# Optimization experiments

Hardware: AMD Instinct MI355X
Metric: run time of the kernel (lower is better)

The kernel has to match this reference:

```python
import jax, jax.numpy as jnp
import numpy as np

V, E, P, T = 65536, 4096, 4096, 512
SENT = 1e9    # finite sentinel for masked min/max (keeps grads NaN-free)
BIG = 1e30    # 'never the minimum' sentinel for invalid points


def setup_inputs() -> dict:
    key = jax.random.key(0)
    k1, k2, k3, k4 = jax.random.split(key, 4)
    verts = jax.random.uniform(k1, (V, 3), dtype=jnp.float32)
    e0 = jax.random.randint(k2, (E,), 0, V - 1)
    edges = jnp.stack([e0, e0 + 1], axis=1)          # distinct endpoints
    listAll = jax.random.randint(k3, (P,), 0, V)
    TableR = jax.random.uniform(k4, (T, 7), dtype=jnp.float32)
    return {"verts": verts, "TableR": TableR, "edges": edges,
            "listAll": listAll, "epoch": 1, "pth": 0}


def _mouth_loss(verts, TableR, edges, listAll):
    v2 = verts[:, :2]                 # deleteaxeZ
    p = v2[listAll]                   # [P,2] query points
    px, py = p[:, 0], p[:, 1]
    ev = v2[edges]                    # [E,2,2]
    x0, y0 = ev[:, 0, 0], ev[:, 0, 1]
    x1, y1 = ev[:, 1, 0], ev[:, 1, 1]
    a = (y0 - y1) / (x0 - x1)         # edge line y = a*x + b (order-invariant)
    b = y0 - a * x0

    # getexpose: first edge with min_x < px < max_x (falls back to last edge)
    xmn, xmx = jnp.minimum(x0, x1), jnp.maximum(x0, x1)
    condA = (px[:, None] > xmn[None, :]) & (px[:, None] < xmx[None, :])  # [P,E]
    idx = jnp.where(condA.any(1), jnp.argmax(condA, axis=1), E - 1)
    exposeY = a[idx] * px + b[idx]
    L1 = jnp.sqrt((py - exposeY) ** 2)        # expose shares x with p -> dx=0
    cy = (py + exposeY) * 0.5                 # centre1 = midpoint (cx == px)
    cx = px

    # getpoints: intersections of horizontal ray y=cy with every edge
    ymn, ymx = jnp.minimum(y0, y1), jnp.maximum(y0, y1)
    condB = (cy[:, None] > ymn[None, :]) & (cy[:, None] < ymx[None, :])  # [P,E]
    xi = (cy[:, None] - b[None, :]) / a[None, :]                          # [P,E]
    n = condB.sum(1)
    xall_mx = jnp.max(jnp.where(condB, xi, -SENT), axis=1)
    xall_mn = jnp.min(jnp.where(condB, xi, SENT), axis=1)
    spu = condB & (xi >= cx[:, None])   # right side (incl. equal, per original)
    inf_ = condB & (xi < cx[:, None])   # left side
    xs = jnp.min(jnp.where(spu, xi, SENT), axis=1)    # minimum of spu
    xinf = jnp.max(jnp.where(inf_, xi, -SENT), axis=1)  # maximum of inf
    has_both = spu.any(1) & inf_.any(1)
    valid = (n == 2) | ((n > 2) & has_both)
    dx = jnp.where(n == 2, xall_mx - xall_mn, xs - xinf)
    L2 = jnp.sqrt(dx ** 2)                    # both points share y=cy
    d1 = jnp.sqrt((cy - 1.0) ** 2)            # dist([1, cy], Ref=(1,1))
    d2 = jnp.sqrt((px - 1.0) ** 2)            # dist([px, 1], Ref=(1,1))

    # al vs every table row (only columns 3..6 are used by the original)
    al = (jnp.abs(L1[:, None] - TableR[None, :, 3])
          + jnp.abs(L2[:, None] - TableR[None, :, 4])
          + jnp.abs(d1[:, None] - TableR[None, :, 5])
          + jnp.abs(d2[:, None] - TableR[None, :, 6]))          # [P,T]
    pm = jnp.min(al, axis=1)                  # per-point best table match
    # `error` is never reset in the original -> running min across points
    m = jnp.where(valid, pm, BIG)
    run = jax.lax.cummin(m, axis=0)
    return jnp.sum(jnp.where(valid, run, 0.0))


def reference(verts, TableR, edges, listAll, epoch, pth):
    # epoch/pth only gate .obj file dumping in the original; no math effect.
    return _mouth_loss(verts, TableR, edges, listAll)
```

## Files before the change

### kernel.cpp

```cpp
#include <hip/hip_runtime.h>
#include <math.h>

#define NV 65536
#define NE 4096
#define NP 4096
#define NT 512
#define NPB 16
#define EW  256
#define SENTF 1000000000.0f
#define BIGF 1e30f

__device__ __forceinline__ float waveMinF(float v) {
    #pragma unroll
    for (int o = 32; o; o >>= 1) v = fminf(v, __shfl_xor(v, o, 64));
    return v;
}
__device__ __forceinline__ int waveMinI(int v) {
    #pragma unroll
    for (int o = 32; o; o >>= 1) v = min(v, __shfl_xor(v, o, 64));
    return v;
}

__global__ void prep_kernel(const float* __restrict__ verts,
                            const int*   __restrict__ edges,
                            const float* __restrict__ tab,
                            float*  __restrict__ ea,  float*  __restrict__ eb,
                            float2* __restrict__ pk2, float4* __restrict__ pk4,
                            float4* __restrict__ tb4) {
    int e = blockIdx.x * blockDim.x + threadIdx.x;
    if (e < NT) {
        const float* r = tab + 7 * e;
        tb4[e] = make_float4(r[3], r[4], r[5], r[6]);
    }
    if (e >= NE) return;
    int i0 = edges[2 * e + 0];
    int i1 = edges[2 * e + 1];
    float x0 = verts[3 * i0 + 0], y0 = verts[3 * i0 + 1];
    float x1 = verts[3 * i1 + 0], y1 = verts[3 * i1 + 1];
    float a = (y0 - y1) / (x0 - x1);
    float b = y0 - a * x0;
    ea[e] = a; eb[e] = b;
    pk2[e] = make_float2(fminf(x0, x1), fmaxf(x0, x1));
    pk4[e] = make_float4(fminf(y0, y1), fmaxf(y0, y1), 1.0f / a, b);
}

__global__ __launch_bounds__(1024) void point_kernel(
        const float*  __restrict__ verts,
        const int*    __restrict__ listAll,
        const float*  __restrict__ ea,  const float*  __restrict__ eb,
        const float2* __restrict__ pk2, const float4* __restrict__ pk4,
        const float4* __restrict__ tb4,
        float* __restrict__ mOut, int* __restrict__ vOut) {
    __shared__ float4 sE[NE];
    __shared__ float  sW[16][NPB][5];
    __shared__ float  sF[NPB][5];
    __shared__ float  sCY[NPB], sPX[NPB], sL1[NPB], sL2[NPB];
    __shared__ int    sVal[NPB];

    const int tid  = threadIdx.x;
    const int lane = tid & 63;
    const int w    = tid >> 6;
    const int pBase = blockIdx.x * NPB;

    float4 r0 = pk4[tid];
    float4 r1 = pk4[1024 + tid];
    float4 r2 = pk4[2048 + tid];
    float4 r3 = pk4[3072 + tid];

    {
        int p  = pBase + w;
        int vi = listAll[p];
        float px = verts[3 * vi + 0];
        float py = verts[3 * vi + 1];
        int minIdx = NE;
        for (int it = 0; it < NE / 64; ++it) {
            int e = it * 64 + lane;
            float2 q = pk2[e];
            bool hit = (px > q.x) && (px < q.y);
            if (hit) minIdx = e;
            if (__any(hit)) break;
        }
        minIdx = waveMinI(minIdx);
        int idx = (minIdx >= NE) ? (NE - 1) : minIdx;
        float exposeY = ea[idx] * px + eb[idx];
        if (lane == 0) {
            sCY[w] = 0.5f * (py + exposeY);
            sL1[w] = fabsf(py - exposeY);
            sPX[w] = px;
        }
    }

    sE[tid]        = r0;
    sE[1024 + tid] = r1;
    sE[2048 + tid] = r2;
    sE[3072 + tid] = r3;
    __syncthreads();

    const int   pl  = lane >> 2;
    const int   s   = lane & 3;
    const float cyl = sCY[pl];
    const float cxl = sPX[pl];

    int   nAcc = 0, hasS = 0, hasI = 0;
    float xallmx = -SENTF, xallmn = SENTF;
    float xs = SENTF, xinf = -SENTF;
    #pragma unroll 8
    for (int k = 0; k < EW / 4; ++k) {
        float4 q4 = sE[w * EW + k * 4 + s];
        bool  c  = (cyl > q4.x) && (cyl < q4.y);
        float xi = (cyl - q4.w) * q4.z;
        nAcc += c ? 1 : 0;
        xallmx = fmaxf(xallmx, c ? xi : -SENTF);
        xallmn = fminf(xallmn, c ? xi :  SENTF);
        bool sp  = c && (xi >= cxl);
        bool in_ = c && (xi <  cxl);
        xs   = fminf(xs,   sp  ? xi :  SENTF);
        xinf = fmaxf(xinf, in_ ? xi : -SENTF);
        hasS |= sp ? 1 : 0;
        hasI |= in_ ? 1 : 0;
    }

    int packed = nAcc | (hasS << 16) | (hasI << 24);
    #pragma unroll
    for (int o = 1; o <= 2; o <<= 1) {
        xallmx = fmaxf(xallmx, __shfl_xor(xallmx, o, 64));
        xallmn = fminf(xallmn, __shfl_xor(xallmn, o, 64));
        xs     = fminf(xs,     __shfl_xor(xs,     o, 64));
        xinf   = fmaxf(xinf,   __shfl_xor(xinf,   o, 64));
        packed += __shfl_xor(packed, o, 64);
    }
    if (s == 0) {
        sW[w][pl][0] = xallmx;
        sW[w][pl][1] = xallmn;
        sW[w][pl][2] = xs;
        sW[w][pl][3] = xinf;
        sW[w][pl][4] = __int_as_float(packed);
    }
    __syncthreads();

    if (tid < 80) {
        int pp = tid & 15, st = tid >> 4;
        if (st == 0) {
            float a0 = sW[0][pp][0];
            #pragma unroll
            for (int ww = 1; ww < 16; ++ww) a0 = fmaxf(a0, sW[ww][pp][0]);
            sF[pp][0] = a0;
        } else if (st == 1) {
            float a0 = sW[0][pp][1];
            #pragma unroll
            for (int ww = 1; ww < 16; ++ww) a0 = fminf(a0, sW[ww][pp][1]);
            sF[pp][1] = a0;
        } else if (st == 2) {
            float a0 = sW[0][pp][2];
            #pragma unroll
            for (int ww = 1; ww < 16; ++ww) a0 = fminf(a0, sW[ww][pp][2]);
            sF[pp][2] = a0;
        } else if (st == 3) {
            float a0 = sW[0][pp][3];
            #pragma unroll
            for (int ww = 1; ww < 16; ++ww) a0 = fmaxf(a0, sW[ww][pp][3]);
            sF[pp][3] = a0;
        } else {
            int a0 = __float_as_int(sW[0][pp][4]);
            #pragma unroll
            for (int ww = 1; ww < 16; ++ww) a0 += __float_as_int(sW[ww][pp][4]);
            sF[pp][4] = __int_as_float(a0);
        }
    }
    __syncthreads();

    if (tid < NPB) {
        int pn = __float_as_int(sF[tid][4]);
        int n  = pn & 0xFFFF;
        int hS = (pn >> 16) & 0xFF;
        int hI = (pn >> 24) & 0xFF;
        bool valid = (n == 2) || ((n > 2) && (hS > 0) && (hI > 0));
        float dx = (n == 2) ? (sF[tid][0] - sF[tid][1]) : (sF[tid][2] - sF[tid][3]);
        sL2[tid]  = fabsf(dx);
        sVal[tid] = valid ? 1 : 0;
    }
    __syncthreads();

    {
        float L1v = sL1[w], L2v = sL2[w];
        float d1  = fabsf(sCY[w] - 1.0f);
        float d2  = fabsf(sPX[w] - 1.0f);
        float pm = INFINITY;
        #pragma unroll
        for (int kk = 0; kk < NT / 64; ++kk) {
            float4 r = tb4[kk * 64 + lane];
            float al = fabsf(L1v - r.x) + fabsf(L2v - r.y) +
                       fabsf(d1 - r.z) + fabsf(d2 - r.w);
            pm = fminf(pm, al);
        }
        pm = waveMinF(pm);
        if (lane == 0) {
            mOut[pBase + w] = sVal[w] ? pm : BIGF;
            vOut[pBase + w] = sVal[w];
        }
    }
}

__global__ __launch_bounds__(1024) void scan_kernel(const float* __restrict__ m,
                                                    const int*   __restrict__ valid,
                                                    float* __restrict__ out) {
    __shared__ float wAgg[16];
    __shared__ float wSum[16];
    int t = threadIdx.x;
    int lane = t & 63, wid = t >> 6;

    float v[4]; int vl[4];
    #pragma unroll
    for (int j = 0; j < 4; j++) { v[j] = m[4 * t + j]; vl[j] = valid[4 * t + j]; }
    float cmin = fminf(fminf(v[0], v[1]), fminf(v[2], v[3]));

    float inc = cmin;
    #pragma unroll
    for (int o = 1; o < 64; o <<= 1) {
        float u = __shfl_up(inc, o, 64);
        if (lane >= o) inc = fminf(inc, u);
    }
    if (lane == 63) wAgg[wid] = inc;
    __syncthreads();

    float wavePrefix = INFINITY;
    for (int i = 0; i < wid; i++) wavePrefix = fminf(wavePrefix, wAgg[i]);
    float excl = __shfl_up(inc, 1, 64);
    if (lane == 0) excl = INFINITY;
    float run = fminf(wavePrefix, excl);

    float sum = 0.0f;
    #pragma unroll
    for (int j = 0; j < 4; j++) {
        run = fminf(run, v[j]);
        if (vl[j]) sum += run;
    }
    #pragma unroll
    for (int o = 32; o; o >>= 1) sum += __shfl_xor(sum, o, 64);
    if (lane == 0) wSum[wid] = sum;
    __syncthreads();
    if (t == 0) {
        float s = 0.0f;
        for (int i = 0; i < 16; i++) s += wSum[i];
        out[0] = s;
    }
}

extern "C" void kernel_launch(void* const* d_in, const int* in_sizes, int n_in,
                              void* d_out, int out_size, void* d_ws, size_t ws_size,
                              hipStream_t stream) {
    const float* verts   = (const float*)d_in[0];
    const float* tab     = (const float*)d_in[1];
    const int*   edges   = (const int*)d_in[2];
    const int*   listAll = (const int*)d_in[3];

    char* ws = (char*)d_ws;
    float4* pk4 = (float4*)ws;                    ws += NE * sizeof(float4);
    float4* tb4 = (float4*)ws;                    ws += NT * sizeof(float4);
    float2* pk2 = (float2*)ws;                    ws += NE * sizeof(float2);
    float*  ea  = (float*)ws;                     ws += NE * sizeof(float);
    float*  eb  = (float*)ws;                     ws += NE * sizeof(float);
    float*  mArr= (float*)ws;                     ws += NP * sizeof(float);
    int*    vArr= (int*)ws;

    prep_kernel<<<(NE + 255) / 256, 256, 0, stream>>>(verts, edges, tab,
                                                      ea, eb, pk2, pk4, tb4);
    point_kernel<<<NP / NPB, 1024, 0, stream>>>(verts, listAll,
                                                ea, eb, pk2, pk4, tb4,
                                                mArr, vArr);
    scan_kernel<<<1, 1024, 0, stream>>>(mArr, vArr, (float*)d_out);
}
```

Measured before the change: 29.37 us.

## Shrink point blocks to four points and stream edges from global without LDS staging

The point kernel now uses 256-thread blocks that each handle 4 points instead of 1024-thread blocks handling 16. Each thread reads edge records straight from global memory (L2-resident) and tests them against all 4 points held in registers. This drops the 64KB LDS staging of all edges per block and the bulky two-level shared reduction. Per-point results are combined with full-wave shuffles plus a small cross-wave combine. The trade-off is four times as many blocks, each re-reading the whole edge table from cache, with less reuse per load than the old 16-point blocks.

```diff
diff --git a/kernel.cpp b/kernel.cpp
--- a/kernel.cpp
+++ b/kernel.cpp
@@ -5,14 +5,22 @@
 #define NE 4096
 #define NP 4096
 #define NT 512
-#define NPB 16
-#define EW  256
 #define SENTF 1000000000.0f
 #define BIGF 1e30f
 
 __device__ __forceinline__ float waveMinF(float v) {
     #pragma unroll
     for (int o = 32; o; o >>= 1) v = fminf(v, __shfl_xor(v, o, 64));
+    return v;
+}
+__device__ __forceinline__ float waveMaxF(float v) {
+    #pragma unroll
+    for (int o = 32; o; o >>= 1) v = fmaxf(v, __shfl_xor(v, o, 64));
+    return v;
+}
+__device__ __forceinline__ int waveSumI(int v) {
+    #pragma unroll
+    for (int o = 32; o; o >>= 1) v += __shfl_xor(v, o, 64);
     return v;
 }
 __device__ __forceinline__ int waveMinI(int v) {
@@ -44,28 +52,22 @@
     pk4[e] = make_float4(fminf(y0, y1), fmaxf(y0, y1), 1.0f / a, b);
 }
 
-__global__ __launch_bounds__(1024) void point_kernel(
+__global__ __launch_bounds__(256) void point_kernel(
         const float*  __restrict__ verts,
         const int*    __restrict__ listAll,
         const float*  __restrict__ ea,  const float*  __restrict__ eb,
         const float2* __restrict__ pk2, const float4* __restrict__ pk4,
         const float4* __restrict__ tb4,
         float* __restrict__ mOut, int* __restrict__ vOut) {
-    __shared__ float4 sE[NE];
-    __shared__ float  sW[16][NPB][5];
-    __shared__ float  sF[NPB][5];
-    __shared__ float  sCY[NPB], sPX[NPB], sL1[NPB], sL2[NPB];
-    __shared__ int    sVal[NPB];
+    __shared__ float sCY[4], sPX[4], sL1[4], sL2[4];
+    __shared__ float sQ[4][4][6];
+    __shared__ float sF[4][6];
+    __shared__ int   sVal[4];
 
     const int tid  = threadIdx.x;
     const int lane = tid & 63;
     const int w    = tid >> 6;
-    const int pBase = blockIdx.x * NPB;
-
-    float4 r0 = pk4[tid];
-    float4 r1 = pk4[1024 + tid];
-    float4 r2 = pk4[2048 + tid];
-    float4 r3 = pk4[3072 + tid];
+    const int pBase = blockIdx.x * 4;
 
     {
         int p  = pBase + w;
@@ -89,91 +91,73 @@
             sPX[w] = px;
         }
     }
-
-    sE[tid]        = r0;
-    sE[1024 + tid] = r1;
-    sE[2048 + tid] = r2;
-    sE[3072 + tid] = r3;
-    __syncthreads();
-
-    const int   pl  = lane >> 2;
-    const int   s   = lane & 3;
-    const float cyl = sCY[pl];
-    const float cxl = sPX[pl];
-
-    int   nAcc = 0, hasS = 0, hasI = 0;
-    float xallmx = -SENTF, xallmn = SENTF;
-    float xs = SENTF, xinf = -SENTF;
-    #pragma unroll 8
-    for (int k = 0; k < EW / 4; ++k) {
-        float4 q4 = sE[w * EW + k * 4 + s];
-        bool  c  = (cyl > q4.x) && (cyl < q4.y);
-        float xi = (cyl - q4.w) * q4.z;
-        nAcc += c ? 1 : 0;
-        xallmx = fmaxf(xallmx, c ? xi : -SENTF);
-        xallmn = fminf(xallmn, c ? xi :  SENTF);
-        bool sp  = c && (xi >= cxl);
-        bool in_ = c && (xi <  cxl);
-        xs   = fminf(xs,   sp  ? xi :  SENTF);
-        xinf = fmaxf(xinf, in_ ? xi : -SENTF);
-        hasS |= sp ? 1 : 0;
-        hasI |= in_ ? 1 : 0;
-    }
-
-    int packed = nAcc | (hasS << 16) | (hasI << 24);
-    #pragma unroll
-    for (int o = 1; o <= 2; o <<= 1) {
-        xallmx = fmaxf(xallmx, __shfl_xor(xallmx, o, 64));
-        xallmn = fminf(xallmn, __shfl_xor(xallmn, o, 64));
-        xs     = fminf(xs,     __shfl_xor(xs,     o, 64));
-        xinf   = fmaxf(xinf,   __shfl_xor(xinf,   o, 64));
-        packed += __shfl_xor(packed, o, 64);
-    }
-    if (s == 0) {
-        sW[w][pl][0] = xallmx;
-        sW[w][pl][1] = xallmn;
-        sW[w][pl][2] = xs;
-        sW[w][pl][3] = xinf;
-        sW[w][pl][4] = __int_as_float(packed);
-    }
-    __syncthreads();
-
-    if (tid < 80) {
-        int pp = tid & 15, st = tid >> 4;
-        if (st == 0) {
-            float a0 = sW[0][pp][0];
-            #pragma unroll
-            for (int ww = 1; ww < 16; ++ww) a0 = fmaxf(a0, sW[ww][pp][0]);
-            sF[pp][0] = a0;
-        } else if (st == 1) {
-            float a0 = sW[0][pp][1];
-            #pragma unroll
-            for (int ww = 1; ww < 16; ++ww) a0 = fminf(a0, sW[ww][pp][1]);
-            sF[pp][1] = a0;
-        } else if (st == 2) {
-            float a0 = sW[0][pp][2];
-            #pragma unroll
-            for (int ww = 1; ww < 16; ++ww) a0 = fminf(a0, sW[ww][pp][2]);
-            sF[pp][2] = a0;
-        } else if (st == 3) {
-            float a0 = sW[0][pp][3];
-            #pragma unroll
-            for (int ww = 1; ww < 16; ++ww) a0 = fmaxf(a0, sW[ww][pp][3]);
-            sF[pp][3] = a0;
-        } else {
-            int a0 = __float_as_int(sW[0][pp][4]);
-            #pragma unroll
-            for (int ww = 1; ww < 16; ++ww) a0 += __float_as_int(sW[ww][pp][4]);
-            sF[pp][4] = __int_as_float(a0);
-        }
-    }
-    __syncthreads();
-
-    if (tid < NPB) {
-        int pn = __float_as_int(sF[tid][4]);
-        int n  = pn & 0xFFFF;
-        int hS = (pn >> 16) & 0xFF;
-        int hI = (pn >> 24) & 0xFF;
+    __syncthreads();
+
+    float cyv[4], cxv[4];
+    #pragma unroll
+    for (int p = 0; p < 4; ++p) { cyv[p] = sCY[p]; cxv[p] = sPX[p]; }
+
+    float mx[4], mn[4], xs[4], xf[4];
+    int   nC[4], hh[4];
+    #pragma unroll
+    for (int p = 0; p < 4; ++p) {
+        mx[p] = -SENTF; mn[p] = SENTF; xs[p] = SENTF; xf[p] = -SENTF;
+        nC[p] = 0; hh[p] = 0;
+    }
+
+    #pragma unroll 4
+    for (int it = 0; it < 16; ++it) {
+        float4 q = pk4[w * 1024 + it * 64 + lane];
+        #pragma unroll
+        for (int p = 0; p < 4; ++p) {
+            float cy = cyv[p], cx = cxv[p];
+            bool  c  = (cy > q.x) && (cy < q.y);
+            float xi = (cy - q.w) * q.z;
+            nC[p] += c ? 1 : 0;
+            mx[p] = fmaxf(mx[p], c ? xi : -SENTF);
+            mn[p] = fminf(mn[p], c ? xi :  SENTF);
+            bool sp  = c && (xi >= cx);
+            bool in_ = c && (xi <  cx);
+            xs[p] = fminf(xs[p], sp  ? xi :  SENTF);
+            xf[p] = fmaxf(xf[p], in_ ? xi : -SENTF);
+            hh[p] |= (sp ? 1 : 0) | (in_ ? 0x10000 : 0);
+        }
+    }
+
+    #pragma unroll
+    for (int p = 0; p < 4; ++p) {
+        float a0 = waveMaxF(mx[p]);
+        float a1 = waveMinF(mn[p]);
+        float a2 = waveMinF(xs[p]);
+        float a3 = waveMaxF(xf[p]);
+        int   a4 = waveSumI(nC[p]);
+        int   a5 = waveSumI(hh[p]);
+        if (lane == 0) {
+            sQ[w][p][0] = a0; sQ[w][p][1] = a1;
+            sQ[w][p][2] = a2; sQ[w][p][3] = a3;
+            sQ[w][p][4] = __int_as_float(a4);
+            sQ[w][p][5] = __int_as_float(a5);
+        }
+    }
+    __syncthreads();
+
+    if (tid < 24) {
+        int p = tid & 3, s = tid >> 2;
+        if (s == 0)      sF[p][0] = fmaxf(fmaxf(sQ[0][p][0], sQ[1][p][0]), fmaxf(sQ[2][p][0], sQ[3][p][0]));
+        else if (s == 1) sF[p][1] = fminf(fminf(sQ[0][p][1], sQ[1][p][1]), fminf(sQ[2][p][1], sQ[3][p][1]));
+        else if (s == 2) sF[p][2] = fminf(fminf(sQ[0][p][2], sQ[1][p][2]), fminf(sQ[2][p][2], sQ[3][p][2]));
+        else if (s == 3) sF[p][3] = fmaxf(fmaxf(sQ[0][p][3], sQ[1][p][3]), fmaxf(sQ[2][p][3], sQ[3][p][3]));
+        else if (s == 4) sF[p][4] = __int_as_float(__float_as_int(sQ[0][p][4]) + __float_as_int(sQ[1][p][4])
+                                                 + __float_as_int(sQ[2][p][4]) + __float_as_int(sQ[3][p][4]));
+        else             sF[p][5] = __int_as_float(__float_as_int(sQ[0][p][5]) + __float_as_int(sQ[1][p][5])
+                                                 + __float_as_int(sQ[2][p][5]) + __float_as_int(sQ[3][p][5]));
+    }
+    __syncthreads();
+
+    if (tid < 4) {
+        int n  = __float_as_int(sF[tid][4]);
+        int hc = __float_as_int(sF[tid][5]);
+        int hS = hc & 0xFFFF, hI = hc >> 16;
         bool valid = (n == 2) || ((n > 2) && (hS > 0) && (hI > 0));
         float dx = (n == 2) ? (sF[tid][0] - sF[tid][1]) : (sF[tid][2] - sF[tid][3]);
         sL2[tid]  = fabsf(dx);
@@ -265,8 +249,8 @@
 
     prep_kernel<<<(NE + 255) / 256, 256, 0, stream>>>(verts, edges, tab,
                                                       ea, eb, pk2, pk4, tb4);
-    point_kernel<<<NP / NPB, 1024, 0, stream>>>(verts, listAll,
-                                                ea, eb, pk2, pk4, tb4,
-                                                mArr, vArr);
+    point_kernel<<<NP / 4, 256, 0, stream>>>(verts, listAll,
+                                             ea, eb, pk2, pk4, tb4,
+                                             mArr, vArr);
     scan_kernel<<<1, 1024, 0, stream>>>(mArr, vArr, (float*)d_out);
 }
```

Measured after the change: 27.50 us, median of 2. 6.4% less time.
